# Performance work log

Measured on AMD Instinct MI355X. Metric: run time of the kernel, lower is better.

Reference implementation:

```python
import jax, jax.numpy as jnp
import numpy as np

SQ, B, H, D = 2048, 1, 16, 64
HIDDEN = H * D


def setup_inputs() -> dict:
    key = jax.random.key(0)
    kq, kk, kv = jax.random.split(key, 3)
    query_layer = jax.random.normal(kq, (SQ, B, H, D), dtype=jnp.float32)
    key_layer = jax.random.normal(kk, (SQ, B, H, D), dtype=jnp.float32)
    value_layer = jax.random.normal(kv, (SQ, B, H, D), dtype=jnp.float32)
    return {"query_layer": query_layer, "key_layer": key_layer, "value_layer": value_layer}


def reference(query_layer, key_layer, value_layer):
    sq, b, h, d = query_layer.shape
    sk = key_layer.shape[0]
    norm = 1.0 / jnp.sqrt(jnp.asarray(d, dtype=query_layer.dtype))
    # scores: [b, h, sq, sk]  (materialized in the original via baddbmm)
    scores = jnp.einsum('sbhd,tbhd->bhst', query_layer, key_layer) * norm
    # causal mask (tril over [sq, sk]); masked positions -> -10000.0 as in original
    causal = jnp.tril(jnp.ones((sq, sk), dtype=bool))
    scores = jnp.where(causal[None, None], scores, jnp.asarray(-10000.0, scores.dtype))
    probs = jax.nn.softmax(scores, axis=-1)
    # context: [sq, b, h, d] -> [sq, b, hidden]
    ctx = jnp.einsum('bhst,tbhd->sbhd', probs, value_layer)
    return ctx.reshape(sq, b, h * d)
```

## Files before the change

kernel.cpp:

```cpp
#include <hip/hip_runtime.h>

typedef __bf16 bf16_t;
typedef bf16_t bf16x4 __attribute__((ext_vector_type(4)));
typedef bf16_t bf16x8 __attribute__((ext_vector_type(8)));
typedef float f32x4 __attribute__((ext_vector_type(4)));
typedef float f32x16 __attribute__((ext_vector_type(16)));

namespace {
constexpr int kNH  = 16;
constexpr int kHD  = 64;
constexpr int kHID = kNH * kHD;
constexpr int kKP  = 72;
constexpr int oQ = 0;
constexpr int oK = 32 * kKP;
constexpr int kSmBytes = 35840;
constexpr int kOmPitch = 68;
}

__global__ __launch_bounds__(256, 2)
void fattn_kernel(const float* __restrict__ Qg, const float* __restrict__ Kg,
                  const float* __restrict__ Vg, float* __restrict__ Og) {
  __shared__ __align__(16) unsigned char smraw[kSmBytes];
  bf16_t* sm = (bf16_t*)smraw;

  const int bid  = blockIdx.x;
  const int head = bid & (kNH - 1);
  const int mt   = 63 - (bid >> 4);
  const int m0   = mt * 32;

  const int tid  = threadIdx.x;
  const int wave = tid >> 6;
  const int lane = tid & 63;
  const int h    = lane >> 5;
  const int m31  = lane & 31;

  bf16_t* qs = sm + oQ;
  bf16_t* ks = sm + oK + wave * 32 * kKP;

  const float kQScale = 0.125f * 1.44269504088896340736f;

  #pragma unroll
  for (int i = 0; i < 2; ++i) {
    const int idx = tid + 256 * i;
    const int row = idx >> 4;
    const int c4  = (idx & 15) * 4;
    const float4 f = *(const float4*)(Qg + (size_t)(m0 + row) * kHID + head * kHD + c4);
    bf16x4 hq;
    hq[0] = (bf16_t)(f.x * kQScale); hq[1] = (bf16_t)(f.y * kQScale);
    hq[2] = (bf16_t)(f.z * kQScale); hq[3] = (bf16_t)(f.w * kQScale);
    *(bf16x4*)(qs + row * kKP + c4) = hq;
  }
  __syncthreads();

  bf16x8 qf[4];
  #pragma unroll
  for (int t = 0; t < 4; ++t)
    qf[t] = *(const bf16x8*)(qs + m31 * kKP + 16 * t + 8 * h);

  f32x16 Oa0, Oa1;
  #pragma unroll
  for (int r = 0; r < 16; ++r) { Oa0[r] = 0.f; Oa1[r] = 0.f; }
  float lacc = 0.f;

  const int krow0 = lane >> 4;
  const int kc4   = (lane & 15) * 4;
  const float* kbase = Kg + head * kHD + kc4;
  const float* vbase = Vg + head * kHD + (size_t)(4 * h) * kHID + m31;

  float4 kreg[8];
  float  vv[32];

  if (wave <= mt) {
    const int kv0 = wave * 32;
    #pragma unroll
    for (int i = 0; i < 8; ++i)
      kreg[i] = *(const float4*)(kbase + (size_t)(kv0 + krow0 + 4 * i) * kHID);
    const float* vt0 = vbase + (size_t)kv0 * kHID;
    #pragma unroll
    for (int db = 0; db < 2; ++db)
      #pragma unroll
      for (int tp = 0; tp < 2; ++tp)
        #pragma unroll
        for (int j = 0; j < 8; ++j)
          vv[db * 16 + tp * 8 + j] =
              vt0[(size_t)(16 * tp + (j & 3) + 8 * (j >> 2)) * kHID + 32 * db];
  }

  for (int jt = wave; jt <= mt; jt += 4) {
    #pragma unroll
    for (int i = 0; i < 8; ++i) {
      bf16x4 hk;
      hk[0] = (bf16_t)kreg[i].x; hk[1] = (bf16_t)kreg[i].y;
      hk[2] = (bf16_t)kreg[i].z; hk[3] = (bf16_t)kreg[i].w;
      *(bf16x4*)(ks + (krow0 + 4 * i) * kKP + kc4) = hk;
    }

    bf16x8 va0, va1, va2, va3;
    #pragma unroll
    for (int j = 0; j < 8; ++j) {
      va0[j] = (bf16_t)vv[j];
      va1[j] = (bf16_t)vv[8 + j];
      va2[j] = (bf16_t)vv[16 + j];
      va3[j] = (bf16_t)vv[24 + j];
    }

    if (jt + 4 <= mt) {
      const int kn = (jt + 4) * 32;
      #pragma unroll
      for (int i = 0; i < 8; ++i)
        kreg[i] = *(const float4*)(kbase + (size_t)(kn + krow0 + 4 * i) * kHID);
      const float* vt0 = vbase + (size_t)kn * kHID;
      #pragma unroll
      for (int db = 0; db < 2; ++db)
        #pragma unroll
        for (int tp = 0; tp < 2; ++tp)
          #pragma unroll
          for (int j = 0; j < 8; ++j)
            vv[db * 16 + tp * 8 + j] =
                vt0[(size_t)(16 * tp + (j & 3) + 8 * (j >> 2)) * kHID + 32 * db];
    }

    f32x16 cs;
    #pragma unroll
    for (int r = 0; r < 16; ++r) cs[r] = 0.f;
    #pragma unroll
    for (int t = 0; t < 4; ++t) {
      bf16x8 af = *(const bf16x8*)(ks + m31 * kKP + 16 * t + 8 * h);
      cs = __builtin_amdgcn_mfma_f32_32x32x16_bf16(af, qf[t], cs, 0, 0, 0);
    }

    float p[16];
    if (jt == mt) {
      #pragma unroll
      for (int r = 0; r < 16; ++r) {
        const int kr = (r & 3) + 8 * (r >> 2) + 4 * h;
        const float x = __builtin_amdgcn_exp2f(cs[r]);
        p[r] = (kr <= m31) ? x : 0.f;
        lacc += p[r];
      }
    } else {
      #pragma unroll
      for (int r = 0; r < 16; ++r) {
        p[r] = __builtin_amdgcn_exp2f(cs[r]);
        lacc += p[r];
      }
    }

    bf16x8 pb0, pb1;
    #pragma unroll
    for (int j = 0; j < 8; ++j) { pb0[j] = (bf16_t)p[j]; pb1[j] = (bf16_t)p[8 + j]; }

    Oa0 = __builtin_amdgcn_mfma_f32_32x32x16_bf16(va0, pb0, Oa0, 0, 0, 0);
    Oa1 = __builtin_amdgcn_mfma_f32_32x32x16_bf16(va2, pb0, Oa1, 0, 0, 0);
    Oa0 = __builtin_amdgcn_mfma_f32_32x32x16_bf16(va1, pb1, Oa0, 0, 0, 0);
    Oa1 = __builtin_amdgcn_mfma_f32_32x32x16_bf16(va3, pb1, Oa1, 0, 0, 0);
  }

  __syncthreads();
  float* fv   = (float*)smraw;
  float* Om   = fv + wave * 32 * kOmPitch;
  float* larr = fv + 4 * 32 * kOmPitch;

  #pragma unroll
  for (int md = 0; md < 2; ++md) {
    const f32x16& Oa = md ? Oa1 : Oa0;
    #pragma unroll
    for (int q = 0; q < 4; ++q) {
      f32x4 v;
      v[0] = Oa[4 * q + 0]; v[1] = Oa[4 * q + 1];
      v[2] = Oa[4 * q + 2]; v[3] = Oa[4 * q + 3];
      *(f32x4*)(Om + (size_t)m31 * kOmPitch + 32 * md + 8 * q + 4 * h) = v;
    }
  }
  larr[wave * 64 + lane] = lacc;
  __syncthreads();

  const int row = tid >> 3;
  const int c0  = (tid & 7) * 8;
  float l = 0.f;
  #pragma unroll
  for (int w = 0; w < 4; ++w)
    l += larr[w * 64 + row] + larr[w * 64 + row + 32];
  const float inv = 1.f / l;

  f32x4 o0, o1;
  #pragma unroll
  for (int e = 0; e < 4; ++e) { o0[e] = 0.f; o1[e] = 0.f; }
  #pragma unroll
  for (int w = 0; w < 4; ++w) {
    const float* src = fv + w * 32 * kOmPitch + (size_t)row * kOmPitch + c0;
    f32x4 a = *(const f32x4*)(src);
    f32x4 b = *(const f32x4*)(src + 4);
    #pragma unroll
    for (int e = 0; e < 4; ++e) { o0[e] += a[e]; o1[e] += b[e]; }
  }
  #pragma unroll
  for (int e = 0; e < 4; ++e) { o0[e] *= inv; o1[e] *= inv; }

  float* dst = Og + (size_t)(m0 + row) * kHID + head * kHD + c0;
  *(f32x4*)(dst)     = o0;
  *(f32x4*)(dst + 4) = o1;
}

extern "C" void kernel_launch(void* const* d_in, const int* in_sizes, int n_in,
                              void* d_out, int out_size, void* d_ws, size_t ws_size,
                              hipStream_t stream) {
  (void)in_sizes; (void)n_in; (void)d_ws; (void)ws_size; (void)out_size;
  const float* Q = (const float*)d_in[0];
  const float* K = (const float*)d_in[1];
  const float* V = (const float*)d_in[2];
  float* O = (float*)d_out;
  dim3 grid(1024);
  dim3 block(256);
  hipLaunchKernelGGL(fattn_kernel, grid, block, 0, stream, Q, K, V, O);
}
```

Baseline: 97.05 us.

## Raise occupancy target, drop K prefetch registers, and balance causal tile order

```diff
diff --git a/kernel.cpp b/kernel.cpp
--- a/kernel.cpp
+++ b/kernel.cpp
@@ -13,11 +13,11 @@
 constexpr int kKP  = 72;
 constexpr int oQ = 0;
 constexpr int oK = 32 * kKP;
+constexpr int kOmPitch = 68;
 constexpr int kSmBytes = 35840;
-constexpr int kOmPitch = 68;
 }
 
-__global__ __launch_bounds__(256, 2)
+__global__ __launch_bounds__(256, 4)
 void fattn_kernel(const float* __restrict__ Qg, const float* __restrict__ Kg,
                   const float* __restrict__ Vg, float* __restrict__ Og) {
   __shared__ __align__(16) unsigned char smraw[kSmBytes];
@@ -25,8 +25,13 @@
 
   const int bid  = blockIdx.x;
   const int head = bid & (kNH - 1);
-  const int mt   = 63 - (bid >> 4);
-  const int m0   = mt * 32;
+  const int q16  = bid >> 4;
+  const int g    = q16 >> 4;
+  const int i16  = q16 & 15;
+  const int mblk = (g == 0) ? (63 - i16) : (g == 1) ? i16
+                 : (g == 2) ? (47 - i16) : (16 + i16);
+  const int m0   = mblk * 32;
+  const int mtk  = mblk;
 
   const int tid  = threadIdx.x;
   const int wave = tid >> 6;
@@ -52,11 +57,6 @@
   }
   __syncthreads();
 
-  bf16x8 qf[4];
-  #pragma unroll
-  for (int t = 0; t < 4; ++t)
-    qf[t] = *(const bf16x8*)(qs + m31 * kKP + 16 * t + 8 * h);
-
   f32x16 Oa0, Oa1;
   #pragma unroll
   for (int r = 0; r < 16; ++r) { Oa0[r] = 0.f; Oa1[r] = 0.f; }
@@ -67,15 +67,10 @@
   const float* kbase = Kg + head * kHD + kc4;
   const float* vbase = Vg + head * kHD + (size_t)(4 * h) * kHID + m31;
 
-  float4 kreg[8];
-  float  vv[32];
-
-  if (wave <= mt) {
-    const int kv0 = wave * 32;
-    #pragma unroll
-    for (int i = 0; i < 8; ++i)
-      kreg[i] = *(const float4*)(kbase + (size_t)(kv0 + krow0 + 4 * i) * kHID);
-    const float* vt0 = vbase + (size_t)kv0 * kHID;
+  float vv[32];
+
+  if (wave <= mtk) {
+    const float* vt0 = vbase + (size_t)(wave * 32) * kHID;
     #pragma unroll
     for (int db = 0; db < 2; ++db)
       #pragma unroll
@@ -86,14 +81,8 @@
               vt0[(size_t)(16 * tp + (j & 3) + 8 * (j >> 2)) * kHID + 32 * db];
   }
 
-  for (int jt = wave; jt <= mt; jt += 4) {
-    #pragma unroll
-    for (int i = 0; i < 8; ++i) {
-      bf16x4 hk;
-      hk[0] = (bf16_t)kreg[i].x; hk[1] = (bf16_t)kreg[i].y;
-      hk[2] = (bf16_t)kreg[i].z; hk[3] = (bf16_t)kreg[i].w;
-      *(bf16x4*)(ks + (krow0 + 4 * i) * kKP + kc4) = hk;
-    }
+  for (int jt = wave; jt <= mtk; jt += 4) {
+    const int kv0 = jt * 32;
 
     bf16x8 va0, va1, va2, va3;
     #pragma unroll
@@ -104,12 +93,8 @@
       va3[j] = (bf16_t)vv[24 + j];
     }
 
-    if (jt + 4 <= mt) {
-      const int kn = (jt + 4) * 32;
-      #pragma unroll
-      for (int i = 0; i < 8; ++i)
-        kreg[i] = *(const float4*)(kbase + (size_t)(kn + krow0 + 4 * i) * kHID);
-      const float* vt0 = vbase + (size_t)kn * kHID;
+    if (jt + 4 <= mtk) {
+      const float* vt0 = vbase + (size_t)((jt + 4) * 32) * kHID;
       #pragma unroll
       for (int db = 0; db < 2; ++db)
         #pragma unroll
@@ -120,36 +105,48 @@
                 vt0[(size_t)(16 * tp + (j & 3) + 8 * (j >> 2)) * kHID + 32 * db];
     }
 
+    #pragma unroll
+    for (int b = 0; b < 2; ++b) {
+      float4 kr[4];
+      #pragma unroll
+      for (int i = 0; i < 4; ++i)
+        kr[i] = *(const float4*)(kbase + (size_t)(kv0 + krow0 + 4 * (4 * b + i)) * kHID);
+      #pragma unroll
+      for (int i = 0; i < 4; ++i) {
+        bf16x4 hk;
+        hk[0] = (bf16_t)kr[i].x; hk[1] = (bf16_t)kr[i].y;
+        hk[2] = (bf16_t)kr[i].z; hk[3] = (bf16_t)kr[i].w;
+        *(bf16x4*)(ks + (krow0 + 4 * (4 * b + i)) * kKP + kc4) = hk;
+      }
+    }
+
     f32x16 cs;
     #pragma unroll
     for (int r = 0; r < 16; ++r) cs[r] = 0.f;
     #pragma unroll
     for (int t = 0; t < 4; ++t) {
       bf16x8 af = *(const bf16x8*)(ks + m31 * kKP + 16 * t + 8 * h);
-      cs = __builtin_amdgcn_mfma_f32_32x32x16_bf16(af, qf[t], cs, 0, 0, 0);
+      bf16x8 qf = *(const bf16x8*)(qs + m31 * kKP + 16 * t + 8 * h);
+      cs = __builtin_amdgcn_mfma_f32_32x32x16_bf16(af, qf, cs, 0, 0, 0);
     }
 
     float p[16];
-    if (jt == mt) {
+    if (jt == mtk) {
       #pragma unroll
       for (int r = 0; r < 16; ++r) {
         const int kr = (r & 3) + 8 * (r >> 2) + 4 * h;
-        const float x = __builtin_amdgcn_exp2f(cs[r]);
-        p[r] = (kr <= m31) ? x : 0.f;
+        const float e = __builtin_amdgcn_exp2f(cs[r]);
+        p[r] = (kr <= m31) ? e : 0.f;
         lacc += p[r];
       }
     } else {
       #pragma unroll
-      for (int r = 0; r < 16; ++r) {
-        p[r] = __builtin_amdgcn_exp2f(cs[r]);
-        lacc += p[r];
-      }
+      for (int r = 0; r < 16; ++r) { p[r] = __builtin_amdgcn_exp2f(cs[r]); lacc += p[r]; }
     }
 
     bf16x8 pb0, pb1;
     #pragma unroll
     for (int j = 0; j < 8; ++j) { pb0[j] = (bf16_t)p[j]; pb1[j] = (bf16_t)p[8 + j]; }
-
     Oa0 = __builtin_amdgcn_mfma_f32_32x32x16_bf16(va0, pb0, Oa0, 0, 0, 0);
     Oa1 = __builtin_amdgcn_mfma_f32_32x32x16_bf16(va2, pb0, Oa1, 0, 0, 0);
     Oa0 = __builtin_amdgcn_mfma_f32_32x32x16_bf16(va1, pb1, Oa0, 0, 0, 0);
@@ -167,8 +164,8 @@
     #pragma unroll
     for (int q = 0; q < 4; ++q) {
       f32x4 v;
-      v[0] = Oa[4 * q + 0]; v[1] = Oa[4 * q + 1];
-      v[2] = Oa[4 * q + 2]; v[3] = Oa[4 * q + 3];
+      #pragma unroll
+      for (int e = 0; e < 4; ++e) v[e] = Oa[4 * q + e];
       *(f32x4*)(Om + (size_t)m31 * kOmPitch + 32 * md + 8 * q + 4 * h) = v;
     }
   }
@@ -180,7 +177,7 @@
   float l = 0.f;
   #pragma unroll
   for (int w = 0; w < 4; ++w)
-    l += larr[w * 64 + row] + larr[w * 64 + row + 32];
+    l += larr[w * 64 + row] + larr[w * 64 + 32 + row];
   const float inv = 1.f / l;
 
   f32x4 o0, o1;
```

Result: slower. 108.3 us (+11.6%).
